# Optimization experiments

Hardware: AMD Instinct MI355X
Metric: run time of the kernel (lower is better)

Reference implementation:

```python
import jax, jax.numpy as jnp
import numpy as np

NUM_HEADS = 4
SPATIAL_DS = 2
EPS = 1e-5


def setup_inputs() -> dict:
    key = jax.random.key(0)
    ks = jax.random.split(key, 6)
    B, C, H, W = 8, 256, 64, 64
    hd = C // NUM_HEADS
    return {
        "x": jax.random.normal(ks[0], (B, C, H, W), jnp.float32),
        "gn_w": jnp.ones((C,), jnp.float32),
        "gn_b": jnp.zeros((C,), jnp.float32),
        "wq": jax.random.normal(ks[1], (C, C), jnp.float32) * (C ** -0.5),
        "wk": jax.random.normal(ks[2], (hd, C), jnp.float32) * (C ** -0.5),
        "wv": jax.random.normal(ks[3], (hd, C), jnp.float32) * (C ** -0.5),
        "wo": jax.random.normal(ks[4], (C, C), jnp.float32) * (C ** -0.5),
        "gamma": jnp.full((C,), 1e-4, jnp.float32),
    }


def reference(x, gn_w, gn_b, wq, wk, wv, wo, gamma):
    B, C, H, W = x.shape
    hd = C // NUM_HEADS
    scale = hd ** -0.5
    ds = SPATIAL_DS

    # GroupNorm with 1 group: normalize over (C,H,W) per sample, per-channel affine
    mu = jnp.mean(x, axis=(1, 2, 3), keepdims=True)
    var = jnp.var(x, axis=(1, 2, 3), keepdims=True)
    xn = (x - mu) * jax.lax.rsqrt(var + EPS)
    xn = xn * gn_w[None, :, None, None] + gn_b[None, :, None, None]

    # Q projection (1x1 conv == channel matmul): (B, heads, N, hd)
    q = jnp.einsum('oc,bchw->bohw', wq, xn).reshape(B, NUM_HEADS, hd, H * W)
    q = jnp.swapaxes(q, 2, 3)  # (B, h, N, hd)

    # AvgPool2d(ds, ds) on normalized input for K/V
    Hd, Wd = H // ds, W // ds
    x_ds = xn.reshape(B, C, Hd, ds, Wd, ds).mean(axis=(3, 5))

    k = jnp.einsum('oc,bchw->bohw', wk, x_ds).reshape(B, hd, Hd * Wd)
    k = jnp.swapaxes(k, 1, 2)  # (B, M, hd) single shared head
    v = jnp.einsum('oc,bchw->bohw', wv, x_ds).reshape(B, hd, Hd * Wd)
    v = jnp.swapaxes(v, 1, 2)  # (B, M, hd)

    # Multi-query attention: queries per-head, shared K/V
    attn = jnp.einsum('bhnd,bmd->bhnm', q, k) * scale
    attn = jax.nn.softmax(attn, axis=-1)
    out = jnp.einsum('bhnm,bmd->bhnd', attn, v)  # (B, h, N, hd)

    out = jnp.swapaxes(out, 2, 3).reshape(B, C, H, W)
    out = jnp.einsum('oc,bchw->bohw', wo, out)

    return x + out * gamma[None, :, None, None]
```

## Files before the change

### kernel.cpp

```cpp
#include <hip/hip_runtime.h>


#define CNT_INV (1.0f/1048576.0f)
#define EPSV 1e-5f
#define QSCALE 0.18033688f

#define WS_STATS 0
#define WS_XNT   64
#define WS_XDS   4194368
#define WS_K     5242944
#define WS_V     5505088
#define WS_WQB   5767232
#define WS_WKV   5800000
#define WS_WOB   5816384

typedef __attribute__((ext_vector_type(8))) short bf8_t;
typedef __attribute__((ext_vector_type(4))) float f4_t;

static __device__ __forceinline__ unsigned fbits(float f) {
  union { float f; unsigned u; } v; v.f = f; return v.u;
}
static __device__ __forceinline__ unsigned short f2bf(float f) {
  unsigned u = fbits(f);
  return (unsigned short)((u + 0x7fffu + ((u >> 16) & 1u)) >> 16);
}
static __device__ __forceinline__ unsigned pk_rnd(float a, float b) {
  return __builtin_amdgcn_perm(fbits(b) + 0x8000u, fbits(a) + 0x8000u, 0x07060302u);
}
static __device__ __forceinline__ unsigned pk_tr(float a, float b) {
  return __builtin_amdgcn_perm(fbits(b), fbits(a), 0x07060302u);
}
static __device__ __forceinline__ float bf2f(unsigned short h) {
  union { unsigned u; float f; } v; v.u = ((unsigned)h) << 16; return v.f;
}
static __device__ __forceinline__ float fexp2(float x) {
  float r; asm("v_exp_f32 %0, %1" : "=v"(r) : "v"(x)); return r;
}

__global__ __launch_bounds__(256) void k_prep_stats(const float* __restrict__ x,
                                                    const float* __restrict__ wq,
                                                    const float* __restrict__ wk,
                                                    const float* __restrict__ wv,
                                                    const float* __restrict__ wo,
                                                    float* __restrict__ stats,
                                                    unsigned short* __restrict__ wqb,
                                                    unsigned short* __restrict__ wkvb,
                                                    unsigned short* __restrict__ wob) {
  const int blk = blockIdx.x;
  const int t = threadIdx.x;
  if (blk < 512) {
    const int b = blk >> 6;
    const int chunk = blk & 63;
    const float4* xb = (const float4*)(x + (size_t)b * 1048576 + (size_t)chunk * 16384);
    float s = 0.f, s2 = 0.f;
#pragma unroll
    for (int it = 0; it < 16; ++it) {
      float4 v = xb[it * 256 + t];
      s  += v.x + v.y + v.z + v.w;
      s2 += v.x * v.x + v.y * v.y + v.z * v.z + v.w * v.w;
    }
#pragma unroll
    for (int o = 32; o > 0; o >>= 1) {
      s  += __shfl_down(s, o);
      s2 += __shfl_down(s2, o);
    }
    __shared__ float red[8];
    const int wid = t >> 6;
    if ((t & 63) == 0) { red[wid] = s; red[4 + wid] = s2; }
    __syncthreads();
    if (t == 0) {
      atomicAdd(&stats[b * 2 + 0], red[0] + red[1] + red[2] + red[3]);
      atomicAdd(&stats[b * 2 + 1], red[4] + red[5] + red[6] + red[7]);
    }
  } else {
    const int idx = (blk - 512) * 256 + t;
    if (idx < 65536) wqb[idx] = f2bf(wq[idx]);
    else if (idx < 81920) wkvb[idx - 65536] = f2bf(wk[idx - 65536]);
    else if (idx < 98304) wkvb[idx - 65536] = f2bf(wv[idx - 81920]);
    else if (idx < 163840) wob[idx - 98304] = f2bf(wo[idx - 98304]);
  }
}

__global__ __launch_bounds__(256) void k_xnt(const float* __restrict__ x,
                                             const float* __restrict__ gnw,
                                             const float* __restrict__ gnb,
                                             const float* __restrict__ stats,
                                             unsigned short* __restrict__ xnT,
                                             unsigned short* __restrict__ xdsT) {
  __shared__ unsigned short T[128][72];
  const int t = threadIdx.x;
  const int b = blockIdx.z, c0 = blockIdx.y * 64, hp = blockIdx.x;
  const int n0 = hp * 128;
  const float mu = stats[b * 2 + 0] * CNT_INV;
  const float rstd = rsqrtf(stats[b * 2 + 1] * CNT_INV - mu * mu + EPSV);
  const int n4 = (t & 31) * 4, cl = t >> 5;
#pragma unroll
  for (int p = 0; p < 8; ++p) {
    const int c = c0 + p * 8 + cl;
    const float gw = gnw[c] * rstd;
    const float gb = gnb[c] - mu * rstd * gnw[c];
    float4 v = *(const float4*)&x[(size_t)(b * 256 + c) * 4096 + n0 + n4];
    T[n4 + 0][p * 8 + cl] = f2bf(v.x * gw + gb);
    T[n4 + 1][p * 8 + cl] = f2bf(v.y * gw + gb);
    T[n4 + 2][p * 8 + cl] = f2bf(v.z * gw + gb);
    T[n4 + 3][p * 8 + cl] = f2bf(v.w * gw + gb);
  }
  __syncthreads();
  {
    const int r = t >> 1, ch = (t & 1) * 32;
    unsigned short* dst = xnT + ((size_t)b * 4096 + n0 + r) * 256 + c0 + ch;
#pragma unroll
    for (int u = 0; u < 4; ++u)
      *(uint4*)(dst + u * 8) = *(const uint4*)&T[r][ch + u * 8];
  }
  {
    const int wd = t & 31, c8 = (t >> 5) * 8;
    uint4 u0 = *(const uint4*)&T[2 * wd][c8];
    uint4 u1 = *(const uint4*)&T[2 * wd + 1][c8];
    uint4 u2 = *(const uint4*)&T[64 + 2 * wd][c8];
    uint4 u3 = *(const uint4*)&T[64 + 2 * wd + 1][c8];
    const unsigned* p0 = (const unsigned*)&u0; const unsigned* p1 = (const unsigned*)&u1;
    const unsigned* p2 = (const unsigned*)&u2; const unsigned* p3 = (const unsigned*)&u3;
    unsigned outp[4];
#pragma unroll
    for (int i = 0; i < 4; ++i) {
      float lo = (bf2f((unsigned short)p0[i]) + bf2f((unsigned short)p1[i]) +
                  bf2f((unsigned short)p2[i]) + bf2f((unsigned short)p3[i])) * 0.25f;
      float hi = (bf2f((unsigned short)(p0[i] >> 16)) + bf2f((unsigned short)(p1[i] >> 16)) +
                  bf2f((unsigned short)(p2[i] >> 16)) + bf2f((unsigned short)(p3[i] >> 16))) * 0.25f;
      outp[i] = pk_rnd(lo, hi);
    }
    *(uint4*)(xdsT + ((size_t)b * 1024 + hp * 32 + wd) * 256 + c0 + c8) = *(uint4*)outp;
  }
}

__global__ __launch_bounds__(256) void k_gemm_kv(const unsigned short* __restrict__ wkvb,
                                                 const unsigned short* __restrict__ xdsT,
                                                 unsigned short* __restrict__ kbf,
                                                 unsigned short* __restrict__ vtbf) {
  const int t = threadIdx.x;
  const int w = t >> 6, l = t & 63, lane16 = l & 15, quad = l >> 4;
  const int m0 = blockIdx.x * 64, b = blockIdx.y;
  const unsigned short* Abase = wkvb + (size_t)(w * 32 + lane16) * 256 + quad * 8;
  const unsigned short* Bbase = xdsT + ((size_t)b * 1024 + m0 + lane16) * 256 + quad * 8;
  f4_t acc[2][4];
#pragma unroll
  for (int i = 0; i < 2; ++i)
#pragma unroll
    for (int j = 0; j < 4; ++j) acc[i][j] = (f4_t){0.f, 0.f, 0.f, 0.f};
  bf8_t Ac[2], Bc[4];
#pragma unroll
  for (int og = 0; og < 2; ++og) Ac[og] = *(const bf8_t*)(Abase + (size_t)og * 16 * 256);
#pragma unroll
  for (int mg = 0; mg < 4; ++mg) Bc[mg] = *(const bf8_t*)(Bbase + (size_t)mg * 16 * 256);
  for (int kc = 0; kc < 256; kc += 32) {
    const int kn = (kc + 32) & 255;
    bf8_t An[2], Bn[4];
#pragma unroll
    for (int og = 0; og < 2; ++og) An[og] = *(const bf8_t*)(Abase + (size_t)og * 16 * 256 + kn);
#pragma unroll
    for (int mg = 0; mg < 4; ++mg) Bn[mg] = *(const bf8_t*)(Bbase + (size_t)mg * 16 * 256 + kn);
#pragma unroll
    for (int og = 0; og < 2; ++og)
#pragma unroll
      for (int mg = 0; mg < 4; ++mg)
        acc[og][mg] = __builtin_amdgcn_mfma_f32_16x16x32_bf16(Ac[og], Bc[mg], acc[og][mg], 0, 0, 0);
#pragma unroll
    for (int og = 0; og < 2; ++og) Ac[og] = An[og];
#pragma unroll
    for (int mg = 0; mg < 4; ++mg) Bc[mg] = Bn[mg];
  }
  if (w < 2) {
#pragma unroll
    for (int og = 0; og < 2; ++og)
#pragma unroll
      for (int mg = 0; mg < 4; ++mg) {
        const int m = m0 + mg * 16 + lane16;
        uint2 p;
        p.x = pk_rnd(acc[og][mg][0], acc[og][mg][1]);
        p.y = pk_rnd(acc[og][mg][2], acc[og][mg][3]);
        *(uint2*)(kbf + (size_t)b * 65536 + (size_t)m * 64 + w * 32 + og * 16 + quad * 4) = p;
      }
  } else {
#pragma unroll
    for (int og = 0; og < 2; ++og)
#pragma unroll
      for (int mg = 0; mg < 4; ++mg) {
        const int m = m0 + mg * 16 + lane16;
        const int d0 = (w - 2) * 32 + og * 16 + quad * 4;
#pragma unroll
        for (int r = 0; r < 4; ++r)
          vtbf[(size_t)b * 65536 + (size_t)(d0 + r) * 1024 + m] = f2bf(acc[og][mg][r]);
      }
  }
}

__global__ __launch_bounds__(256) void k_fused(const unsigned short* __restrict__ wqb,
                                               const unsigned short* __restrict__ xnT,
                                               const unsigned short* __restrict__ kbf,
                                               const unsigned short* __restrict__ vtbf,
                                               const unsigned short* __restrict__ wob,
                                               const float* __restrict__ x,
                                               const float* __restrict__ gamma,
                                               float* __restrict__ outp) {
  __shared__ __align__(16) unsigned short smem[20480];
  const int t = threadIdx.x;
  const int w = t >> 6, l = t & 63, lane16 = l & 15, quad = l >> 4;
  const int n0 = blockIdx.x * 64, b = blockIdx.y;
  const int h = w;
  unsigned short* qst = smem + w * 4608;
  unsigned short (*plds)[64][40] = (unsigned short (*)[64][40])(smem + w * 5120);
  unsigned short (*aos)[264] = (unsigned short (*)[264])smem;

  const unsigned short* kb = kbf + (size_t)b * 65536;
  const unsigned short* vb = vtbf + (size_t)b * 65536;

  {
    const unsigned short* Abase = wqb + (size_t)(h * 64 + lane16) * 256 + quad * 8;
    const unsigned short* Bbase = xnT + ((size_t)b * 4096 + n0 + lane16) * 256 + quad * 8;
    f4_t qacc[4][4];
#pragma unroll
    for (int i = 0; i < 4; ++i)
#pragma unroll
      for (int j = 0; j < 4; ++j) qacc[i][j] = (f4_t){0.f, 0.f, 0.f, 0.f};
    for (int kc = 0; kc < 256; kc += 32) {
      bf8_t A[4], Bf[4];
#pragma unroll
      for (int og = 0; og < 4; ++og) A[og] = *(const bf8_t*)(Abase + (size_t)og * 16 * 256 + kc);
#pragma unroll
      for (int ng = 0; ng < 4; ++ng) Bf[ng] = *(const bf8_t*)(Bbase + (size_t)ng * 16 * 256 + kc);
#pragma unroll
      for (int og = 0; og < 4; ++og)
#pragma unroll
        for (int ng = 0; ng < 4; ++ng)
          qacc[og][ng] = __builtin_amdgcn_mfma_f32_16x16x32_bf16(A[og], Bf[ng], qacc[og][ng], 0, 0, 0);
    }
#pragma unroll
    for (int og = 0; og < 4; ++og)
#pragma unroll
      for (int ng = 0; ng < 4; ++ng) {
        uint2 p;
        p.x = pk_rnd(qacc[og][ng][0] * QSCALE, qacc[og][ng][1] * QSCALE);
        p.y = pk_rnd(qacc[og][ng][2] * QSCALE, qacc[og][ng][3] * QSCALE);
        *(uint2*)&qst[(ng * 16 + lane16) * 72 + og * 16 + quad * 4] = p;
      }
  }
  bf8_t Qf[4][2];
#pragma unroll
  for (int qg = 0; qg < 4; ++qg)
#pragma unroll
    for (int dc = 0; dc < 2; ++dc)
      Qf[qg][dc] = *(const bf8_t*)&qst[(qg * 16 + lane16) * 72 + dc * 32 + quad * 8];
  __syncthreads();

  f4_t O[4][4];
#pragma unroll
  for (int dg = 0; dg < 4; ++dg)
#pragma unroll
    for (int qg = 0; qg < 4; ++qg) O[dg][qg] = (f4_t){0.f, 0.f, 0.f, 0.f};
  float den[4] = {0.f, 0.f, 0.f, 0.f};

#define SSTEP(KREG, BUF)                                                      \
  {                                                                           \
    _Pragma("unroll")                                                         \
    for (int qg = 0; qg < 4; ++qg) {                                          \
      _Pragma("unroll")                                                       \
      for (int s = 0; s < 2; ++s) {                                           \
        f4_t S = (f4_t){0.f, 0.f, 0.f, 0.f};                                  \
        S = __builtin_amdgcn_mfma_f32_16x16x32_bf16(KREG[s][0], Qf[qg][0], S, 0, 0, 0); \
        S = __builtin_amdgcn_mfma_f32_16x16x32_bf16(KREG[s][1], Qf[qg][1], S, 0, 0, 0); \
        float e0 = fexp2(S[0]);                                               \
        float e1 = fexp2(S[1]);                                               \
        float e2 = fexp2(S[2]);                                               \
        float e3 = fexp2(S[3]);                                               \
        den[qg] += (e0 + e1) + (e2 + e3);                                     \
        uint2 p; p.x = pk_tr(e0, e1); p.y = pk_tr(e2, e3);                    \
        *(uint2*)&plds[BUF][qg * 16 + lane16][s * 16 + quad * 4] = p;         \
      }                                                                       \
    }                                                                         \
  }

  bf8_t Kc[2][2];
#pragma unroll
  for (int s = 0; s < 2; ++s)
#pragma unroll
    for (int dc = 0; dc < 2; ++dc)
      Kc[s][dc] = *(const bf8_t*)(kb + (size_t)(s * 16 + lane16) * 64 + dc * 32 + quad * 8);
  SSTEP(Kc, 0);

  bf8_t Vc[4];
#pragma unroll
  for (int s = 0; s < 2; ++s)
#pragma unroll
    for (int dc = 0; dc < 2; ++dc)
      Kc[s][dc] = *(const bf8_t*)(kb + (size_t)(32 + s * 16 + lane16) * 64 + dc * 32 + quad * 8);
#pragma unroll
  for (int dg = 0; dg < 4; ++dg)
    Vc[dg] = *(const bf8_t*)(vb + (size_t)(dg * 16 + lane16) * 1024 + quad * 8);

  for (int it = 1; it < 32; ++it) {
    const int cb = it & 1, pb = cb ^ 1;
    bf8_t Pf[4];
#pragma unroll
    for (int qg = 0; qg < 4; ++qg)
      Pf[qg] = *(const bf8_t*)&plds[pb][qg * 16 + lane16][quad * 8];
    const int kvk = ((it + 1) & 31) * 32;
    const int kvv = it * 32;
    bf8_t K2[2][2], V2[4];
#pragma unroll
    for (int s = 0; s < 2; ++s)
#pragma unroll
      for (int dc = 0; dc < 2; ++dc)
        K2[s][dc] = *(const bf8_t*)(kb + (size_t)(kvk + s * 16 + lane16) * 64 + dc * 32 + quad * 8);
#pragma unroll
    for (int dg = 0; dg < 4; ++dg)
      V2[dg] = *(const bf8_t*)(vb + (size_t)(dg * 16 + lane16) * 1024 + kvv + quad * 8);
#pragma unroll
    for (int dg = 0; dg < 4; ++dg)
#pragma unroll
      for (int qg = 0; qg < 4; ++qg)
        O[dg][qg] = __builtin_amdgcn_mfma_f32_16x16x32_bf16(Vc[dg], Pf[qg], O[dg][qg], 0, 0, 0);
    SSTEP(Kc, cb);
#pragma unroll
    for (int s = 0; s < 2; ++s)
#pragma unroll
      for (int dc = 0; dc < 2; ++dc) Kc[s][dc] = K2[s][dc];
#pragma unroll
    for (int dg = 0; dg < 4; ++dg) Vc[dg] = V2[dg];
  }
  {
    bf8_t Pf[4];
#pragma unroll
    for (int qg = 0; qg < 4; ++qg)
      Pf[qg] = *(const bf8_t*)&plds[1][qg * 16 + lane16][quad * 8];
#pragma unroll
    for (int dg = 0; dg < 4; ++dg)
#pragma unroll
      for (int qg = 0; qg < 4; ++qg)
        O[dg][qg] = __builtin_amdgcn_mfma_f32_16x16x32_bf16(Vc[dg], Pf[qg], O[dg][qg], 0, 0, 0);
  }
#undef SSTEP

  float rden[4];
#pragma unroll
  for (int qg = 0; qg < 4; ++qg) {
    float d = den[qg];
    d += __shfl_xor(d, 16);
    d += __shfl_xor(d, 32);
    rden[qg] = 1.f / d;
  }

  __syncthreads();
#pragma unroll
  for (int dg = 0; dg < 4; ++dg)
#pragma unroll
    for (int qg = 0; qg < 4; ++qg) {
      const int c0 = h * 64 + dg * 16 + quad * 4;
      uint2 p;
      p.x = pk_rnd(O[dg][qg][0] * rden[qg], O[dg][qg][1] * rden[qg]);
      p.y = pk_rnd(O[dg][qg][2] * rden[qg], O[dg][qg][3] * rden[qg]);
      *(uint2*)&aos[qg * 16 + lane16][c0] = p;
    }
  __syncthreads();

  {
    const unsigned short* Wbase = wob + (size_t)(w * 64 + lane16) * 256 + quad * 8;
    f4_t acc[4][4];
#pragma unroll
    for (int i = 0; i < 4; ++i)
#pragma unroll
      for (int j = 0; j < 4; ++j) acc[i][j] = (f4_t){0.f, 0.f, 0.f, 0.f};
    for (int kc = 0; kc < 256; kc += 32) {
      bf8_t A[4], Bf[4];
#pragma unroll
      for (int og = 0; og < 4; ++og) A[og] = *(const bf8_t*)(Wbase + (size_t)og * 16 * 256 + kc);
#pragma unroll
      for (int ng = 0; ng < 4; ++ng) Bf[ng] = *(const bf8_t*)&aos[ng * 16 + lane16][kc + quad * 8];
#pragma unroll
      for (int og = 0; og < 4; ++og)
#pragma unroll
        for (int ng = 0; ng < 4; ++ng)
          acc[og][ng] = __builtin_amdgcn_mfma_f32_16x16x32_bf16(A[og], Bf[ng], acc[og][ng], 0, 0, 0);
    }
#pragma unroll
    for (int og = 0; og < 4; ++og) {
      float4 g4 = *(const float4*)&gamma[w * 64 + og * 16 + quad * 4];
      const float g[4] = {g4.x, g4.y, g4.z, g4.w};
#pragma unroll
      for (int ng = 0; ng < 4; ++ng) {
        const int n = n0 + ng * 16 + lane16;
#pragma unroll
        for (int r = 0; r < 4; ++r) {
          const int o = w * 64 + og * 16 + quad * 4 + r;
          const size_t ix = ((size_t)(b * 256 + o)) * 4096 + n;
          outp[ix] = x[ix] + g[r] * acc[og][ng][r];
        }
      }
    }
  }
}

extern "C" void kernel_launch(void* const* d_in, const int* in_sizes, int n_in,
                              void* d_out, int out_size, void* d_ws, size_t ws_size,
                              hipStream_t stream) {
  const float* x     = (const float*)d_in[0];
  const float* gnw   = (const float*)d_in[1];
  const float* gnb   = (const float*)d_in[2];
  const float* wq    = (const float*)d_in[3];
  const float* wk    = (const float*)d_in[4];
  const float* wv    = (const float*)d_in[5];
  const float* wo    = (const float*)d_in[6];
  const float* gamma = (const float*)d_in[7];
  float* out = (float*)d_out;
  float* ws  = (float*)d_ws;
  unsigned short* xnT  = (unsigned short*)(ws + WS_XNT);
  unsigned short* xdsT = (unsigned short*)(ws + WS_XDS);
  unsigned short* kbf  = (unsigned short*)(ws + WS_K);
  unsigned short* vtbf = (unsigned short*)(ws + WS_V);
  unsigned short* wqb  = (unsigned short*)(ws + WS_WQB);
  unsigned short* wkvb = (unsigned short*)(ws + WS_WKV);
  unsigned short* wob  = (unsigned short*)(ws + WS_WOB);

  hipMemsetAsync(ws, 0, 256, stream);
  k_prep_stats<<<1152, 256, 0, stream>>>(x, wq, wk, wv, wo, ws + WS_STATS, wqb, wkvb, wob);
  k_xnt<<<dim3(32, 4, 8), 256, 0, stream>>>(x, gnw, gnb, ws + WS_STATS, xnT, xdsT);
  k_gemm_kv<<<dim3(16, 8), 256, 0, stream>>>(wkvb, xdsT, kbf, vtbf);
  k_fused<<<dim3(64, 8), 256, 0, stream>>>(wqb, xnT, kbf, vtbf, wob, x, gamma, out);
}
```

Baseline: 215.1 us.

## Unroll attention KV loop by two and replace stats atomics with partials

The attention inner loop now handles 64 keys per iteration with two P buffers, and the score computation writes packed 128-bit LDS stores. V loads are split so the P-fragment key order matches the packed layout. GroupNorm statistics are written as per-block partial sums and reduced inside k_xnt, which removes the hipMemsetAsync and the atomics. This raises register pressure and adds a small redundant reduction in every k_xnt block.

```diff
diff --git a/kernel.cpp b/kernel.cpp
--- a/kernel.cpp
+++ b/kernel.cpp
@@ -6,13 +6,13 @@
 #define QSCALE 0.18033688f
 
 #define WS_STATS 0
-#define WS_XNT   64
-#define WS_XDS   4194368
-#define WS_K     5242944
-#define WS_V     5505088
-#define WS_WQB   5767232
-#define WS_WKV   5800000
-#define WS_WOB   5816384
+#define WS_XNT   1024
+#define WS_XDS   4195328
+#define WS_K     5243904
+#define WS_V     5506048
+#define WS_WQB   5768192
+#define WS_WKV   5800960
+#define WS_WOB   5817344
 
 typedef __attribute__((ext_vector_type(8))) short bf8_t;
 typedef __attribute__((ext_vector_type(4))) float f4_t;
@@ -35,6 +35,12 @@
 }
 static __device__ __forceinline__ float fexp2(float x) {
   float r; asm("v_exp_f32 %0, %1" : "=v"(r) : "v"(x)); return r;
+}
+static __device__ __forceinline__ bf8_t ldV(const unsigned short* p) {
+  union { bf8_t v; uint2 u[2]; } r;
+  r.u[0] = *(const uint2*)p;
+  r.u[1] = *(const uint2*)(p + 16);
+  return r.v;
 }
 
 __global__ __launch_bounds__(256) void k_prep_stats(const float* __restrict__ x,
@@ -69,8 +75,10 @@
     if ((t & 63) == 0) { red[wid] = s; red[4 + wid] = s2; }
     __syncthreads();
     if (t == 0) {
-      atomicAdd(&stats[b * 2 + 0], red[0] + red[1] + red[2] + red[3]);
-      atomicAdd(&stats[b * 2 + 1], red[4] + red[5] + red[6] + red[7]);
+      float2 p;
+      p.x = red[0] + red[1] + red[2] + red[3];
+      p.y = red[4] + red[5] + red[6] + red[7];
+      ((float2*)stats)[blk] = p;
     }
   } else {
     const int idx = (blk - 512) * 256 + t;
@@ -88,11 +96,26 @@
                                              unsigned short* __restrict__ xnT,
                                              unsigned short* __restrict__ xdsT) {
   __shared__ unsigned short T[128][72];
+  __shared__ float mv2[2];
   const int t = threadIdx.x;
   const int b = blockIdx.z, c0 = blockIdx.y * 64, hp = blockIdx.x;
   const int n0 = hp * 128;
-  const float mu = stats[b * 2 + 0] * CNT_INV;
-  const float rstd = rsqrtf(stats[b * 2 + 1] * CNT_INV - mu * mu + EPSV);
+  if (t < 64) {
+    float2 p = ((const float2*)stats)[b * 64 + t];
+    float s = p.x, s2 = p.y;
+#pragma unroll
+    for (int o = 32; o > 0; o >>= 1) {
+      s  += __shfl_down(s, o);
+      s2 += __shfl_down(s2, o);
+    }
+    if (t == 0) {
+      const float mu = s * CNT_INV;
+      mv2[0] = mu;
+      mv2[1] = rsqrtf(s2 * CNT_INV - mu * mu + EPSV);
+    }
+  }
+  __syncthreads();
+  const float mu = mv2[0], rstd = mv2[1];
   const int n4 = (t & 31) * 4, cl = t >> 5;
 #pragma unroll
   for (int p = 0; p < 8; ++p) {
@@ -260,86 +283,95 @@
     for (int qg = 0; qg < 4; ++qg) O[dg][qg] = (f4_t){0.f, 0.f, 0.f, 0.f};
   float den[4] = {0.f, 0.f, 0.f, 0.f};
 
-#define SSTEP(KREG, BUF)                                                      \
-  {                                                                           \
-    _Pragma("unroll")                                                         \
-    for (int qg = 0; qg < 4; ++qg) {                                          \
-      _Pragma("unroll")                                                       \
-      for (int s = 0; s < 2; ++s) {                                           \
-        f4_t S = (f4_t){0.f, 0.f, 0.f, 0.f};                                  \
-        S = __builtin_amdgcn_mfma_f32_16x16x32_bf16(KREG[s][0], Qf[qg][0], S, 0, 0, 0); \
-        S = __builtin_amdgcn_mfma_f32_16x16x32_bf16(KREG[s][1], Qf[qg][1], S, 0, 0, 0); \
-        float e0 = fexp2(S[0]);                                               \
-        float e1 = fexp2(S[1]);                                               \
-        float e2 = fexp2(S[2]);                                               \
-        float e3 = fexp2(S[3]);                                               \
-        den[qg] += (e0 + e1) + (e2 + e3);                                     \
-        uint2 p; p.x = pk_tr(e0, e1); p.y = pk_tr(e2, e3);                    \
-        *(uint2*)&plds[BUF][qg * 16 + lane16][s * 16 + quad * 4] = p;         \
-      }                                                                       \
-    }                                                                         \
-  }
-
-  bf8_t Kc[2][2];
-#pragma unroll
-  for (int s = 0; s < 2; ++s)
-#pragma unroll
-    for (int dc = 0; dc < 2; ++dc)
-      Kc[s][dc] = *(const bf8_t*)(kb + (size_t)(s * 16 + lane16) * 64 + dc * 32 + quad * 8);
-  SSTEP(Kc, 0);
-
-  bf8_t Vc[4];
-#pragma unroll
-  for (int s = 0; s < 2; ++s)
-#pragma unroll
-    for (int dc = 0; dc < 2; ++dc)
-      Kc[s][dc] = *(const bf8_t*)(kb + (size_t)(32 + s * 16 + lane16) * 64 + dc * 32 + quad * 8);
-#pragma unroll
-  for (int dg = 0; dg < 4; ++dg)
-    Vc[dg] = *(const bf8_t*)(vb + (size_t)(dg * 16 + lane16) * 1024 + quad * 8);
-
-  for (int it = 1; it < 32; ++it) {
-    const int cb = it & 1, pb = cb ^ 1;
-    bf8_t Pf[4];
-#pragma unroll
-    for (int qg = 0; qg < 4; ++qg)
-      Pf[qg] = *(const bf8_t*)&plds[pb][qg * 16 + lane16][quad * 8];
-    const int kvk = ((it + 1) & 31) * 32;
-    const int kvv = it * 32;
-    bf8_t K2[2][2], V2[4];
+#define SSTEP2(KU, BUF)                                                        \
+  {                                                                            \
+    _Pragma("unroll")                                                          \
+    for (int qg = 0; qg < 4; ++qg) {                                           \
+      f4_t S0 = (f4_t){0.f, 0.f, 0.f, 0.f};                                    \
+      f4_t S1 = (f4_t){0.f, 0.f, 0.f, 0.f};                                    \
+      S0 = __builtin_amdgcn_mfma_f32_16x16x32_bf16(KU[0][0], Qf[qg][0], S0, 0, 0, 0); \
+      S0 = __builtin_amdgcn_mfma_f32_16x16x32_bf16(KU[0][1], Qf[qg][1], S0, 0, 0, 0); \
+      S1 = __builtin_amdgcn_mfma_f32_16x16x32_bf16(KU[1][0], Qf[qg][0], S1, 0, 0, 0); \
+      S1 = __builtin_amdgcn_mfma_f32_16x16x32_bf16(KU[1][1], Qf[qg][1], S1, 0, 0, 0); \
+      float e0 = fexp2(S0[0]), e1 = fexp2(S0[1]), e2 = fexp2(S0[2]), e3 = fexp2(S0[3]); \
+      float e4 = fexp2(S1[0]), e5 = fexp2(S1[1]), e6 = fexp2(S1[2]), e7 = fexp2(S1[3]); \
+      den[qg] += ((e0 + e1) + (e2 + e3)) + ((e4 + e5) + (e6 + e7));            \
+      uint4 pk;                                                                \
+      pk.x = pk_tr(e0, e1); pk.y = pk_tr(e2, e3);                              \
+      pk.z = pk_tr(e4, e5); pk.w = pk_tr(e6, e7);                              \
+      *(uint4*)&plds[BUF][qg * 16 + lane16][quad * 8] = pk;                    \
+    }                                                                          \
+  }
+
+  bf8_t Kp[2][2][2];
+#pragma unroll
+  for (int u = 0; u < 2; ++u)
 #pragma unroll
     for (int s = 0; s < 2; ++s)
 #pragma unroll
       for (int dc = 0; dc < 2; ++dc)
-        K2[s][dc] = *(const bf8_t*)(kb + (size_t)(kvk + s * 16 + lane16) * 64 + dc * 32 + quad * 8);
+        Kp[u][s][dc] = *(const bf8_t*)(kb + (size_t)(u * 32 + s * 16 + lane16) * 64 + dc * 32 + quad * 8);
+  SSTEP2(Kp[0], 0);
+  SSTEP2(Kp[1], 1);
+
+  bf8_t Vc[2][4], Vn[2][4];
+#pragma unroll
+  for (int u = 0; u < 2; ++u)
 #pragma unroll
     for (int dg = 0; dg < 4; ++dg)
-      V2[dg] = *(const bf8_t*)(vb + (size_t)(dg * 16 + lane16) * 1024 + kvv + quad * 8);
-#pragma unroll
-    for (int dg = 0; dg < 4; ++dg)
+      Vc[u][dg] = ldV(vb + (size_t)(dg * 16 + lane16) * 1024 + u * 32 + quad * 4);
+
+  for (int p = 1; p < 16; ++p) {
+    const int kv0 = p * 64;
+    bf8_t Pf[2][4];
+#pragma unroll
+    for (int u = 0; u < 2; ++u)
 #pragma unroll
       for (int qg = 0; qg < 4; ++qg)
-        O[dg][qg] = __builtin_amdgcn_mfma_f32_16x16x32_bf16(Vc[dg], Pf[qg], O[dg][qg], 0, 0, 0);
-    SSTEP(Kc, cb);
-#pragma unroll
-    for (int s = 0; s < 2; ++s)
-#pragma unroll
-      for (int dc = 0; dc < 2; ++dc) Kc[s][dc] = K2[s][dc];
-#pragma unroll
-    for (int dg = 0; dg < 4; ++dg) Vc[dg] = V2[dg];
+        Pf[u][qg] = *(const bf8_t*)&plds[u][qg * 16 + lane16][quad * 8];
+#pragma unroll
+    for (int u = 0; u < 2; ++u)
+#pragma unroll
+      for (int s = 0; s < 2; ++s)
+#pragma unroll
+        for (int dc = 0; dc < 2; ++dc)
+          Kp[u][s][dc] = *(const bf8_t*)(kb + (size_t)(kv0 + u * 32 + s * 16 + lane16) * 64 + dc * 32 + quad * 8);
+#pragma unroll
+    for (int u = 0; u < 2; ++u)
+#pragma unroll
+      for (int dg = 0; dg < 4; ++dg)
+        Vn[u][dg] = ldV(vb + (size_t)(dg * 16 + lane16) * 1024 + kv0 + u * 32 + quad * 4);
+#pragma unroll
+    for (int u = 0; u < 2; ++u)
+#pragma unroll
+      for (int dg = 0; dg < 4; ++dg)
+#pragma unroll
+        for (int qg = 0; qg < 4; ++qg)
+          O[dg][qg] = __builtin_amdgcn_mfma_f32_16x16x32_bf16(Vc[u][dg], Pf[u][qg], O[dg][qg], 0, 0, 0);
+    SSTEP2(Kp[0], 0);
+    SSTEP2(Kp[1], 1);
+#pragma unroll
+    for (int u = 0; u < 2; ++u)
+#pragma unroll
+      for (int dg = 0; dg < 4; ++dg)
+        Vc[u][dg] = Vn[u][dg];
   }
   {
-    bf8_t Pf[4];
-#pragma unroll
-    for (int qg = 0; qg < 4; ++qg)
-      Pf[qg] = *(const bf8_t*)&plds[1][qg * 16 + lane16][quad * 8];
-#pragma unroll
-    for (int dg = 0; dg < 4; ++dg)
+    bf8_t Pf[2][4];
+#pragma unroll
+    for (int u = 0; u < 2; ++u)
 #pragma unroll
       for (int qg = 0; qg < 4; ++qg)
-        O[dg][qg] = __builtin_amdgcn_mfma_f32_16x16x32_bf16(Vc[dg], Pf[qg], O[dg][qg], 0, 0, 0);
-  }
-#undef SSTEP
+        Pf[u][qg] = *(const bf8_t*)&plds[u][qg * 16 + lane16][quad * 8];
+#pragma unroll
+    for (int u = 0; u < 2; ++u)
+#pragma unroll
+      for (int dg = 0; dg < 4; ++dg)
+#pragma unroll
+        for (int qg = 0; qg < 4; ++qg)
+          O[dg][qg] = __builtin_amdgcn_mfma_f32_16x16x32_bf16(Vc[u][dg], Pf[u][qg], O[dg][qg], 0, 0, 0);
+  }
+#undef SSTEP2
 
   float rden[4];
 #pragma unroll
@@ -421,7 +453,6 @@
   unsigned short* wkvb = (unsigned short*)(ws + WS_WKV);
   unsigned short* wob  = (unsigned short*)(ws + WS_WOB);
 
-  hipMemsetAsync(ws, 0, 256, stream);
   k_prep_stats<<<1152, 256, 0, stream>>>(x, wq, wk, wv, wo, ws + WS_STATS, wqb, wkvb, wob);
   k_xnt<<<dim3(32, 4, 8), 256, 0, stream>>>(x, gnw, gnb, ws + WS_STATS, xnT, xdsT);
   k_gemm_kv<<<dim3(16, 8), 256, 0, stream>>>(wkvb, xdsT, kbf, vtbf);
```

Result: slower. 235.9 us (+9.7%).
